# Optimization experiments

Hardware: AMD Instinct MI355X
Metric: run time of the kernel (lower is better)

## Reference

```python
import jax, jax.numpy as jnp
import numpy as np


def setup_inputs() -> dict:
    key = jax.random.key(0)
    k1, k2, k3, k4 = jax.random.split(key, 4)
    B, S, I, O = 2, 4096, 4096, 4096
    x = jax.random.normal(k1, (B, S, I), dtype=jnp.float32)
    # packed int4 weights: each byte holds two nibbles; [O, I//2]
    qweight = jax.random.randint(k2, (O, I // 2), 0, 256, dtype=jnp.int32)
    # per-tensor weight scale (scalar, stored as shape [1])
    weight_scale = jax.random.uniform(k3, (1,), dtype=jnp.float32) * 0.01 + 1e-3
    bias = jax.random.normal(k4, (O,), dtype=jnp.float32)
    return {"x": x, "qweight": qweight, "weight_scale": weight_scale, "bias": bias}


def _dequant_weight(qweight, weight_scale):
    # unpack_int4 (dim=1): high nibble -> even cols, low nibble -> odd cols
    high = (qweight >> 4) - 8           # [O, I//2], values in [-8, 7]
    low = (qweight & 15) - 8            # [O, I//2]
    unpacked = jnp.stack([high, low], axis=-1).reshape(qweight.shape[0], -1)  # [O, I]
    # no weight_offset -> w = q * scale
    return unpacked.astype(weight_scale.dtype) * weight_scale


def reference(x, qweight, weight_scale, bias):
    w = _dequant_weight(qweight, weight_scale)  # [O, I] fp32
    # dynamic per-tensor symmetric int8 activation quantization
    max_abs = jnp.max(jnp.abs(x))
    scale = max_abs / 127.0
    scale = jnp.where(scale == 0, jnp.ones_like(scale), scale)
    x_dq = jnp.round(x / scale) * scale  # fake-quantized activations (offset = 0)
    # F.linear: x @ w.T + bias
    out = jnp.einsum('bsi,oi->bso', x_dq, w) + bias
    return out.astype(x.dtype)
```

## Files before the change

kernel.cpp:

```cpp
#include <hip/hip_runtime.h>


typedef __attribute__((ext_vector_type(4))) int int32x4;

__device__ __forceinline__ void async_copy16(const void* gsrc, void* ldsdst) {
  __builtin_amdgcn_global_load_lds(
      (const __attribute__((address_space(1))) void*)gsrc,
      (__attribute__((address_space(3))) void*)ldsdst, 16, 0, 0);
}

__global__ void amax_kernel(const float* __restrict__ x,
                            float* __restrict__ partial, int n4) {
  int tid = blockIdx.x * blockDim.x + threadIdx.x;
  int stride = gridDim.x * blockDim.x;
  float m = 0.0f;
  const float4* x4 = (const float4*)x;
  for (int i = tid; i < n4; i += stride) {
    float4 v = x4[i];
    m = fmaxf(m, fmaxf(fmaxf(fabsf(v.x), fabsf(v.y)),
                       fmaxf(fabsf(v.z), fabsf(v.w))));
  }
#pragma unroll
  for (int off = 32; off > 0; off >>= 1)
    m = fmaxf(m, __shfl_down(m, off, 64));
  __shared__ float red[4];
  if ((threadIdx.x & 63) == 0) red[threadIdx.x >> 6] = m;
  __syncthreads();
  if (threadIdx.x == 0) {
    partial[blockIdx.x] = fmaxf(fmaxf(red[0], red[1]), fmaxf(red[2], red[3]));
  }
}

__global__ void amax_reduce(const float* __restrict__ partial,
                            float* __restrict__ amax) {
  const int t = threadIdx.x;
  float m = fmaxf(partial[t], partial[t + 256]);
#pragma unroll
  for (int off = 32; off > 0; off >>= 1)
    m = fmaxf(m, __shfl_down(m, off, 64));
  __shared__ float red[4];
  if ((t & 63) == 0) red[t >> 6] = m;
  __syncthreads();
  if (t == 0)
    *amax = fmaxf(fmaxf(red[0], red[1]), fmaxf(red[2], red[3]));
}

__global__ void quant_kernel(const float* __restrict__ x,
                             const float* __restrict__ amax_p,
                             unsigned* __restrict__ qx, int n4) {
  float s = *amax_p / 127.0f;
  if (s == 0.0f) s = 1.0f;
  const float inv = 1.0f / s;
  int tid = blockIdx.x * blockDim.x + threadIdx.x;
  int stride = gridDim.x * blockDim.x;
  const float4* x4 = (const float4*)x;
  for (int i = tid; i < n4; i += stride) {
    float4 v = x4[i];
    int a = __float2int_rn(v.x * inv);
    int b = __float2int_rn(v.y * inv);
    int c = __float2int_rn(v.z * inv);
    int d = __float2int_rn(v.w * inv);
    qx[i] = (unsigned)(a & 0xFF) | ((unsigned)(b & 0xFF) << 8) |
            ((unsigned)(c & 0xFF) << 16) | ((unsigned)(d & 0xFF) << 24);
  }
}

__device__ __forceinline__ unsigned pack2(int q) {
  unsigned hi = (unsigned)((((q >> 4) & 15) - 8) & 0xFF);
  unsigned lo = (unsigned)(((q & 15) - 8) & 0xFF);
  return hi | (lo << 8);
}

__global__ void repack_kernel(const int* __restrict__ qw,
                              uint2* __restrict__ w8, int n4) {
  int tid = blockIdx.x * blockDim.x + threadIdx.x;
  int stride = gridDim.x * blockDim.x;
  const int4* q4 = (const int4*)qw;
  for (int i = tid; i < n4; i += stride) {
    int4 q = q4[i];
    uint2 r;
    r.x = pack2(q.x) | (pack2(q.y) << 16);
    r.y = pack2(q.z) | (pack2(q.w) << 16);
    w8[i] = r;
  }
}

#define BM 256
#define BN 256
#define BKT 64
#define TILE_B (BM * BKT)

__global__ __launch_bounds__(512, 2) void gemm_i8(
    const char* __restrict__ A, const char* __restrict__ Bt,
    const float* __restrict__ bias, const float* __restrict__ amax_p,
    const float* __restrict__ wscale, float* __restrict__ C,
    int M, int N, int K) {
  __shared__ alignas(16) char As[4 * TILE_B];
  __shared__ alignas(16) char Bs[4 * TILE_B];

  const int tid = threadIdx.x;
  const int lane = tid & 63;
  const int wave = tid >> 6;
  const int wm = wave >> 2;
  const int wn = wave & 3;
  const int quad = lane >> 4;
  const int l16 = lane & 15;

  const int cpx = gridDim.x >> 3;
  const int wg = (blockIdx.x & 7) * cpx + (blockIdx.x >> 3);
  const int bM = (wg >> 4) * BM;
  const int bN = (wg & 15) * BN;

  const int NT = K >> 6;

  const int srow = tid >> 2;
  const int scoff = (((tid & 3) ^ ((tid >> 3) & 3)) << 4);
  const char* aS = A + (size_t)(bM + srow) * K + scoff;
  const char* bS = Bt + (size_t)(bN + srow) * K + scoff;
  const size_t skip = (size_t)128 * K;
  char* aD = &As[tid * 16];
  char* bD = &Bs[tid * 16];

  for (int tt = 0; tt < 3; ++tt) {
    const int boff = tt * TILE_B;
    const char* sa = aS + tt * BKT;
    const char* sb = bS + tt * BKT;
    async_copy16(sa, aD + boff);
    async_copy16(sa + skip, aD + boff + 8192);
    async_copy16(sb, bD + boff);
    async_copy16(sb + skip, bD + boff + 8192);
  }

  const int xsl = ((quad ^ ((l16 >> 1) & 3)) << 4);
  const int arow0 = (wm << 7) + l16;
  const int brow0 = (wn << 6) + l16;

  int32x4 acc[8][4] = {};

  for (int t = 0; t < NT; ++t) {
    if (t + 2 < NT)
      asm volatile("s_waitcnt vmcnt(8)" ::: "memory");
    else if (t + 1 < NT)
      asm volatile("s_waitcnt vmcnt(4)" ::: "memory");
    else
      asm volatile("s_waitcnt vmcnt(0)" ::: "memory");
    __builtin_amdgcn_s_barrier();
    __builtin_amdgcn_sched_barrier(0);

    const char* Ab = &As[(t & 3) * TILE_B];
    const char* Bb = &Bs[(t & 3) * TILE_B];
    const int pboff = ((t + 3) & 3) * TILE_B;
    const bool do_stage = (t + 3 < NT);

    int32x4 af[4], bf[4];

#pragma unroll
    for (int i = 0; i < 4; ++i)
      af[i] = *(const int32x4*)(Ab + (arow0 + i * 16) * BKT + xsl);
#pragma unroll
    for (int j = 0; j < 4; ++j)
      bf[j] = *(const int32x4*)(Bb + (brow0 + j * 16) * BKT + xsl);
    if (do_stage) {
      const char* sa = aS + (t + 3) * BKT;
      async_copy16(sa, aD + pboff);
      async_copy16(sa + skip, aD + pboff + 8192);
    }
    __builtin_amdgcn_s_barrier();
    __builtin_amdgcn_s_setprio(1);
#pragma unroll
    for (int i = 0; i < 4; ++i)
#pragma unroll
      for (int j = 0; j < 4; ++j)
        acc[i][j] = __builtin_amdgcn_mfma_i32_16x16x64_i8(af[i], bf[j],
                                                          acc[i][j], 0, 0, 0);
    __builtin_amdgcn_s_setprio(0);

#pragma unroll
    for (int i = 0; i < 4; ++i)
      af[i] = *(const int32x4*)(Ab + (arow0 + 64 + i * 16) * BKT + xsl);
    if (do_stage) {
      const char* sb = bS + (t + 3) * BKT;
      async_copy16(sb, bD + pboff);
      async_copy16(sb + skip, bD + pboff + 8192);
    }
    __builtin_amdgcn_s_barrier();
    __builtin_amdgcn_s_setprio(1);
#pragma unroll
    for (int i = 0; i < 4; ++i)
#pragma unroll
      for (int j = 0; j < 4; ++j)
        acc[4 + i][j] = __builtin_amdgcn_mfma_i32_16x16x64_i8(
            af[i], bf[j], acc[4 + i][j], 0, 0, 0);
    __builtin_amdgcn_s_setprio(0);
  }

  float s = *amax_p / 127.0f;
  if (s == 0.0f) s = 1.0f;
  const float cs = s * wscale[0];

#pragma unroll
  for (int f = 0; f < 8; ++f) {
#pragma unroll
    for (int j = 0; j < 4; ++j) {
      const int n = bN + (wn << 6) + j * 16 + l16;
#pragma unroll
      for (int r = 0; r < 4; ++r) {
        const int m = bM + (wm << 7) + f * 16 + quad * 4 + r;
        C[(size_t)m * N + n] = (float)acc[f][j][r] * cs + bias[n];
      }
    }
  }
}

extern "C" void kernel_launch(void* const* d_in, const int* in_sizes, int n_in,
                              void* d_out, int out_size, void* d_ws,
                              size_t ws_size, hipStream_t stream) {
  const float* x = (const float*)d_in[0];
  const int* qw = (const int*)d_in[1];
  const float* wscale = (const float*)d_in[2];
  const float* bias = (const float*)d_in[3];
  float* out = (float*)d_out;

  const int nx = in_sizes[0];
  const int npacked = in_sizes[1];
  const int O = in_sizes[3];
  const int I = (npacked / O) * 2;
  const int M = nx / I;

  float* amax = (float*)d_ws;
  float* partial = (float*)((char*)d_ws + 256);
  char* qx = (char*)d_ws + 8192;
  char* w8 = qx + (size_t)nx;

  amax_kernel<<<512, 256, 0, stream>>>(x, partial, nx / 4);
  amax_reduce<<<1, 256, 0, stream>>>(partial, amax);
  quant_kernel<<<2048, 256, 0, stream>>>(x, amax, (unsigned*)qx, nx / 4);
  repack_kernel<<<1024, 256, 0, stream>>>(qw, (uint2*)w8, npacked / 4);

  const int nwg = (M / BM) * (O / BN);
  gemm_i8<<<nwg, 512, 0, stream>>>(qx, w8, bias, amax, wscale, out, M, O, I);
}
```

Before: 406.9 us.

## Fuse amax reduce into quant, switch GEMM to 3-stage pipeline with occupancy 1

Removes the single-block amax_reduce launch by having each quant block redundantly reduce the 1024 partials itself, and doubles the amax grid with a 2-way unrolled load loop. The GEMM's LDS ring shrinks from four stages to three (prefetch distance 2), adds extra barriers and lgkmcnt waits around the MFMA phases, and changes launch bounds to one block per CU. This trades fewer launches and less LDS for a shallower prefetch depth and lower occupancy hint.

```diff
diff --git a/kernel.cpp b/kernel.cpp
--- a/kernel.cpp
+++ b/kernel.cpp
@@ -15,10 +15,14 @@
   int stride = gridDim.x * blockDim.x;
   float m = 0.0f;
   const float4* x4 = (const float4*)x;
-  for (int i = tid; i < n4; i += stride) {
+  for (int i = tid; i < n4; i += 2 * stride) {
     float4 v = x4[i];
+    float4 w = (i + stride < n4) ? x4[i + stride]
+                                 : make_float4(0.f, 0.f, 0.f, 0.f);
     m = fmaxf(m, fmaxf(fmaxf(fabsf(v.x), fabsf(v.y)),
                        fmaxf(fabsf(v.z), fabsf(v.w))));
+    m = fmaxf(m, fmaxf(fmaxf(fabsf(w.x), fabsf(w.y)),
+                       fmaxf(fabsf(w.z), fabsf(w.w))));
   }
 #pragma unroll
   for (int off = 32; off > 0; off >>= 1)
@@ -31,27 +35,31 @@
   }
 }
 
-__global__ void amax_reduce(const float* __restrict__ partial,
-                            float* __restrict__ amax) {
+__global__ void quant_kernel(const float* __restrict__ x,
+                             const float* __restrict__ partial,
+                             float* __restrict__ amax_out,
+                             unsigned* __restrict__ qx, int n4) {
   const int t = threadIdx.x;
-  float m = fmaxf(partial[t], partial[t + 256]);
+  float m = fmaxf(fmaxf(partial[t], partial[t + 256]),
+                  fmaxf(partial[t + 512], partial[t + 768]));
 #pragma unroll
   for (int off = 32; off > 0; off >>= 1)
     m = fmaxf(m, __shfl_down(m, off, 64));
   __shared__ float red[4];
   if ((t & 63) == 0) red[t >> 6] = m;
   __syncthreads();
-  if (t == 0)
-    *amax = fmaxf(fmaxf(red[0], red[1]), fmaxf(red[2], red[3]));
-}
-
-__global__ void quant_kernel(const float* __restrict__ x,
-                             const float* __restrict__ amax_p,
-                             unsigned* __restrict__ qx, int n4) {
-  float s = *amax_p / 127.0f;
-  if (s == 0.0f) s = 1.0f;
-  const float inv = 1.0f / s;
-  int tid = blockIdx.x * blockDim.x + threadIdx.x;
+  __shared__ float s_bcast;
+  if (t == 0) {
+    float amax = fmaxf(fmaxf(red[0], red[1]), fmaxf(red[2], red[3]));
+    if (blockIdx.x == 0) *amax_out = amax;
+    float s = amax / 127.0f;
+    if (s == 0.0f) s = 1.0f;
+    s_bcast = 1.0f / s;
+  }
+  __syncthreads();
+  const float inv = s_bcast;
+
+  int tid = blockIdx.x * blockDim.x + t;
   int stride = gridDim.x * blockDim.x;
   const float4* x4 = (const float4*)x;
   for (int i = tid; i < n4; i += stride) {
@@ -90,13 +98,13 @@
 #define BKT 64
 #define TILE_B (BM * BKT)
 
-__global__ __launch_bounds__(512, 2) void gemm_i8(
+__global__ __launch_bounds__(512, 1) void gemm_i8(
     const char* __restrict__ A, const char* __restrict__ Bt,
     const float* __restrict__ bias, const float* __restrict__ amax_p,
     const float* __restrict__ wscale, float* __restrict__ C,
     int M, int N, int K) {
-  __shared__ alignas(16) char As[4 * TILE_B];
-  __shared__ alignas(16) char Bs[4 * TILE_B];
+  __shared__ alignas(16) char As[3 * TILE_B];
+  __shared__ alignas(16) char Bs[3 * TILE_B];
 
   const int tid = threadIdx.x;
   const int lane = tid & 63;
@@ -118,17 +126,15 @@
   const char* aS = A + (size_t)(bM + srow) * K + scoff;
   const char* bS = Bt + (size_t)(bN + srow) * K + scoff;
   const size_t skip = (size_t)128 * K;
-  char* aD = &As[tid * 16];
-  char* bD = &Bs[tid * 16];
-
-  for (int tt = 0; tt < 3; ++tt) {
+
+  for (int tt = 0; tt < 2; ++tt) {
     const int boff = tt * TILE_B;
     const char* sa = aS + tt * BKT;
     const char* sb = bS + tt * BKT;
-    async_copy16(sa, aD + boff);
-    async_copy16(sa + skip, aD + boff + 8192);
-    async_copy16(sb, bD + boff);
-    async_copy16(sb + skip, bD + boff + 8192);
+    async_copy16(sa, &As[boff] + tid * 16);
+    async_copy16(sa + skip, &As[boff + 8192] + tid * 16);
+    async_copy16(sb, &Bs[boff] + tid * 16);
+    async_copy16(sb + skip, &Bs[boff + 8192] + tid * 16);
   }
 
   const int xsl = ((quad ^ ((l16 >> 1) & 3)) << 4);
@@ -136,23 +142,16 @@
   const int brow0 = (wn << 6) + l16;
 
   int32x4 acc[8][4] = {};
+  int32x4 af[4], bf[4];
+
+  asm volatile("s_waitcnt vmcnt(4)" ::: "memory");
+  __builtin_amdgcn_s_barrier();
+  __builtin_amdgcn_sched_barrier(0);
 
   for (int t = 0; t < NT; ++t) {
-    if (t + 2 < NT)
-      asm volatile("s_waitcnt vmcnt(8)" ::: "memory");
-    else if (t + 1 < NT)
-      asm volatile("s_waitcnt vmcnt(4)" ::: "memory");
-    else
-      asm volatile("s_waitcnt vmcnt(0)" ::: "memory");
-    __builtin_amdgcn_s_barrier();
-    __builtin_amdgcn_sched_barrier(0);
-
-    const char* Ab = &As[(t & 3) * TILE_B];
-    const char* Bb = &Bs[(t & 3) * TILE_B];
-    const int pboff = ((t + 3) & 3) * TILE_B;
-    const bool do_stage = (t + 3 < NT);
-
-    int32x4 af[4], bf[4];
+    const char* Ab = &As[(t % 3) * TILE_B];
+    const char* Bb = &Bs[(t % 3) * TILE_B];
+    const bool st = (t + 2 < NT);
 
 #pragma unroll
     for (int i = 0; i < 4; ++i)
@@ -160,12 +159,15 @@
 #pragma unroll
     for (int j = 0; j < 4; ++j)
       bf[j] = *(const int32x4*)(Bb + (brow0 + j * 16) * BKT + xsl);
-    if (do_stage) {
-      const char* sa = aS + (t + 3) * BKT;
-      async_copy16(sa, aD + pboff);
-      async_copy16(sa + skip, aD + pboff + 8192);
+    if (st) {
+      const char* sa = aS + (t + 2) * BKT;
+      char* ad = &As[((t + 2) % 3) * TILE_B] + tid * 16;
+      async_copy16(sa, ad);
+      async_copy16(sa + skip, ad + 8192);
     }
     __builtin_amdgcn_s_barrier();
+    asm volatile("s_waitcnt lgkmcnt(0)" ::: "memory");
+    __builtin_amdgcn_sched_barrier(0);
     __builtin_amdgcn_s_setprio(1);
 #pragma unroll
     for (int i = 0; i < 4; ++i)
@@ -174,16 +176,20 @@
         acc[i][j] = __builtin_amdgcn_mfma_i32_16x16x64_i8(af[i], bf[j],
                                                           acc[i][j], 0, 0, 0);
     __builtin_amdgcn_s_setprio(0);
+    __builtin_amdgcn_s_barrier();
 
 #pragma unroll
     for (int i = 0; i < 4; ++i)
       af[i] = *(const int32x4*)(Ab + (arow0 + 64 + i * 16) * BKT + xsl);
-    if (do_stage) {
-      const char* sb = bS + (t + 3) * BKT;
-      async_copy16(sb, bD + pboff);
-      async_copy16(sb + skip, bD + pboff + 8192);
+    if (st) {
+      const char* sb = bS + (t + 2) * BKT;
+      char* bd = &Bs[((t + 2) % 3) * TILE_B] + tid * 16;
+      async_copy16(sb, bd);
+      async_copy16(sb + skip, bd + 8192);
     }
     __builtin_amdgcn_s_barrier();
+    asm volatile("s_waitcnt lgkmcnt(0)" ::: "memory");
+    __builtin_amdgcn_sched_barrier(0);
     __builtin_amdgcn_s_setprio(1);
 #pragma unroll
     for (int i = 0; i < 4; ++i)
@@ -192,6 +198,12 @@
         acc[4 + i][j] = __builtin_amdgcn_mfma_i32_16x16x64_i8(
             af[i], bf[j], acc[4 + i][j], 0, 0, 0);
     __builtin_amdgcn_s_setprio(0);
+    if (st)
+      asm volatile("s_waitcnt vmcnt(4)" ::: "memory");
+    else
+      asm volatile("s_waitcnt vmcnt(0)" ::: "memory");
+    __builtin_amdgcn_s_barrier();
+    __builtin_amdgcn_sched_barrier(0);
   }
 
   float s = *amax_p / 127.0f;
@@ -232,9 +244,9 @@
   char* qx = (char*)d_ws + 8192;
   char* w8 = qx + (size_t)nx;
 
-  amax_kernel<<<512, 256, 0, stream>>>(x, partial, nx / 4);
-  amax_reduce<<<1, 256, 0, stream>>>(partial, amax);
-  quant_kernel<<<2048, 256, 0, stream>>>(x, amax, (unsigned*)qx, nx / 4);
+  amax_kernel<<<1024, 256, 0, stream>>>(x, partial, nx / 4);
+  quant_kernel<<<2048, 256, 0, stream>>>(x, partial, amax, (unsigned*)qx,
+                                         nx / 4);
   repack_kernel<<<1024, 256, 0, stream>>>(qw, (uint2*)w8, npacked / 4);
 
   const int nwg = (M / BM) * (O / BN);
```

Measured after the change: 412.0 us. No clear change (+1.2%).
